# Kernel optimization log

Hardware: AMD Instinct MI355X
Metric: run time of the kernel (lower is better)

The kernel has to match this reference:

```python
import jax, jax.numpy as jnp
import numpy as np

N, E, D = 50000, 600000, 128

def _lin(key, fan_in, fan_out):
    kw, kb = jax.random.split(key)
    s = 1.0 / np.sqrt(fan_in)
    W = jax.random.uniform(kw, (fan_in, fan_out), minval=-s, maxval=s, dtype=jnp.float32)
    b = jax.random.uniform(kb, (fan_out,), minval=-s, maxval=s, dtype=jnp.float32)
    return W, b

def setup_inputs() -> dict:
    key = jax.random.key(0)
    ks = jax.random.split(key, 16)
    h = jax.random.normal(ks[0], (N, D), dtype=jnp.float32)
    pos = jax.random.normal(ks[1], (N, 2), dtype=jnp.float32)
    edge_index = jax.random.randint(ks[2], (2, E), 0, N, dtype=jnp.int64)
    edge_attr = jax.random.uniform(ks[3], (E, 1), dtype=jnp.float32)
    Wq, bq = _lin(ks[4], D, D)
    Wk, bk = _lin(ks[5], D, D)
    Wv, bv = _lin(ks[6], D, D)
    We1, be1 = _lin(ks[7], 1, D)
    We2, be2 = _lin(ks[8], D, D)
    Wa1, ba1 = _lin(ks[9], 3 * D, D)
    Wa2, ba2 = _lin(ks[10], D, 1)
    Wm1, bm1 = _lin(ks[11], 2 * D, D)
    Wm2, bm2 = _lin(ks[12], D, D)
    return dict(h=h, pos=pos, edge_index=edge_index, edge_attr=edge_attr,
                Wq=Wq, bq=bq, Wk=Wk, bk=bk, Wv=Wv, bv=bv,
                We1=We1, be1=be1, We2=We2, be2=be2,
                Wa1=Wa1, ba1=ba1, Wa2=Wa2, ba2=ba2,
                Wm1=Wm1, bm1=bm1, Wm2=Wm2, bm2=bm2)

def reference(h, pos, edge_index, edge_attr,
              Wq, bq, Wk, bk, Wv, bv,
              We1, be1, We2, be2,
              Wa1, ba1, Wa2, ba2,
              Wm1, bm1, Wm2, bm2):
    row, col = edge_index[0], edge_index[1]  # source, destination
    q = h @ Wq + bq                          # [N, D]
    k = h @ Wk + bk
    v = h @ Wv + bv
    e = jax.nn.relu(edge_attr @ We1 + be1) @ We2 + be2  # [E, D]
    # per-edge attention logits
    attn_in = jnp.concatenate([q[col], k[row], e], axis=-1)          # [E, 3D]
    logits = (jax.nn.relu(attn_in @ Wa1 + ba1) @ Wa2 + ba2)[:, 0]    # [E]
    # segment softmax grouped by destination node (torch_geometric style)
    seg_max = jax.ops.segment_max(logits, col, num_segments=N)       # [N]
    ex = jnp.exp(logits - seg_max[col])
    seg_sum = jax.ops.segment_sum(ex, col, num_segments=N)           # [N]
    w = ex / (seg_sum[col] + 1e-16)                                  # [E]
    # per-edge messages
    msg_in = jnp.concatenate([v[row], e], axis=-1)                   # [E, 2D]
    msg = jax.nn.silu(msg_in @ Wm1 + bm1) @ Wm2 + bm2                # [E, D]
    agg = jax.ops.segment_sum(msg * w[:, None], col, num_segments=N) # [N, D]
    return (h + agg, pos)
```

## Files before the change

kernel.cpp:

```cpp
#include <hip/hip_runtime.h>
#include <math.h>

#define D 128
#define SB 256

typedef __attribute__((ext_vector_type(8))) short bf16x8;
typedef __attribute__((ext_vector_type(4))) float f32x4;

__device__ inline unsigned f2bf(float f) {
    unsigned u = __float_as_uint(f);
    return (u + 0x7FFFu + ((u >> 16) & 1u)) >> 16;
}

__global__ __launch_bounds__(256) void prep(
    const float* __restrict__ Wq, const float* __restrict__ bq,
    const float* __restrict__ Wk, const float* __restrict__ bk,
    const float* __restrict__ Wv, const float* __restrict__ bv,
    const float* __restrict__ Wa1, const float* __restrict__ ba1,
    const float* __restrict__ Wm1, const float* __restrict__ bm1,
    const float* __restrict__ We1, const float* __restrict__ be1,
    const float* __restrict__ We2, const float* __restrict__ be2,
    const float* __restrict__ Wm2,
    const int* __restrict__ ei, int E,
    ushort* __restrict__ Wpk, ushort* __restrict__ Wpk2,
    float* __restrict__ bqa, float* __restrict__ bka, float* __restrict__ bva,
    float* __restrict__ bounds,
    float2* __restrict__ AB, float2* __restrict__ MB,
    int* __restrict__ deg)
{
    __shared__ float smem[1536];
    int b = blockIdx.x;
    int t = threadIdx.x;
    int j = t & 127, half = t >> 7;
    if (b < 384) {
        int which = b >> 7, i = b & 127;
        const float *A, *B;
        if (which == 0)      { A = Wq; B = Wa1; }
        else if (which == 1) { A = Wk; B = Wa1 + 128 * D; }
        else                 { A = Wv; B = Wm1; }
        float acc = 0.f;
        for (int k = half * 64; k < half * 64 + 64; k++) acc += A[i * D + k] * B[k * D + j];
        smem[t] = acc;
        __syncthreads();
        if (half == 0) {
            float v = smem[j] + smem[128 + j];
            int gc = which * 128 + j;
            int nt = gc >> 4;
            int ks = i >> 5;
            int lane = (((i >> 3) & 3) << 4) | (gc & 15);
            int j8 = i & 7;
            Wpk[((nt * 4 + ks) * 64 + lane) * 8 + j8] = (ushort)f2bf(v);
        }
    } else if (b < 387) {
        int which = b - 384;
        const float *bias, *B, *extra; float *out;
        if (which == 0)      { bias = bq; B = Wa1;           out = bqa; extra = ba1; }
        else if (which == 1) { bias = bk; B = Wa1 + 128 * D; out = bka; extra = nullptr; }
        else                 { bias = bv; B = Wm1;           out = bva; extra = bm1; }
        float acc = 0.f;
        for (int k = half * 64; k < half * 64 + 64; k++) acc += bias[k] * B[k * D + j];
        smem[t] = acc;
        __syncthreads();
        if (half == 0) out[j] = smem[j] + smem[128 + j] + (extra ? extra[j] : 0.f);
    } else if (b == 387) {
        float* sb = smem;
        if (t < 128) {
            float w = We1[t], bb = be1[t];
            float th = (w != 0.f) ? (-bb / w) : 2.f;
            sb[t] = fminf(fmaxf(th, 0.f), 1.f);
        }
        __syncthreads();
        for (int k = 2; k <= 128; k <<= 1)
            for (int jj = k >> 1; jj > 0; jj >>= 1) {
                if (t < 128) {
                    int ixj = t ^ jj;
                    if (ixj > t) {
                        float a = sb[t], c = sb[ixj];
                        bool up = ((t & k) == 0);
                        if (up ? (a > c) : (a < c)) { sb[t] = c; sb[ixj] = a; }
                    }
                }
                __syncthreads();
            }
        if (t == 0) { bounds[0] = 0.f; bounds[129] = 1.f; }
        if (t < 128) bounds[1 + t] = sb[t];
    } else if (b < 517) {
        float* sb = smem;
        float* Ae = smem + 128;
        float* Be = smem + 256;
        float* P  = smem + 384;
        if (t < 128) {
            float w = We1[t], bb = be1[t];
            float th = (w != 0.f) ? (-bb / w) : 2.f;
            sb[t] = fminf(fmaxf(th, 0.f), 1.f);
        }
        __syncthreads();
        for (int k = 2; k <= 128; k <<= 1)
            for (int jj = k >> 1; jj > 0; jj >>= 1) {
                if (t < 128) {
                    int ixj = t ^ jj;
                    if (ixj > t) {
                        float a = sb[t], c = sb[ixj];
                        bool up = ((t & k) == 0);
                        if (up ? (a > c) : (a < c)) { sb[t] = c; sb[ixj] = a; }
                    }
                }
                __syncthreads();
            }
        int i = b - 388;
        float lo = (i == 0)   ? 0.f : sb[i - 1];
        float hi = (i == 128) ? 1.f : sb[i];
        float m = 0.5f * (lo + hi);
        float ae = 0.f, be = 0.f;
        for (int k = half * 64; k < half * 64 + 64; k++) {
            float ww = We1[k], bb2 = be1[k];
            if (m * ww + bb2 > 0.f) { ae += ww * We2[k * D + j]; be += bb2 * We2[k * D + j]; }
        }
        P[t] = ae; P[256 + t] = be;
        __syncthreads();
        if (half == 0) {
            Ae[j] = P[j] + P[128 + j];
            Be[j] = P[256 + j] + P[384 + j] + be2[j];
        }
        __syncthreads();
        float aa = 0.f, ba = 0.f, am = 0.f, bm = 0.f;
        for (int l2 = half * 64; l2 < half * 64 + 64; l2++) {
            float ael = Ae[l2], bel = Be[l2];
            float wa = Wa1[(256 + l2) * D + j];
            float wm = Wm1[(128 + l2) * D + j];
            aa += ael * wa; ba += bel * wa;
            am += ael * wm; bm += bel * wm;
        }
        P[t] = aa; P[256 + t] = ba; P[512 + t] = am; P[768 + t] = bm;
        __syncthreads();
        if (half == 0) {
            AB[i * 128 + j] = make_float2(P[j] + P[128 + j], P[256 + j] + P[384 + j]);
            MB[i * 128 + j] = make_float2(P[512 + j] + P[640 + j], P[768 + j] + P[896 + j]);
        }
    } else if (b < 645) {
        if (t < 128) {
            int i = b - 517;
            int nt = t >> 4;
            int ks = i >> 5;
            int lane = (((i >> 3) & 3) << 4) | (t & 15);
            int j8 = i & 7;
            Wpk2[((nt * 4 + ks) * 64 + lane) * 8 + j8] = (ushort)f2bf(Wm2[i * D + t]);
        }
    } else {
        int e = (b - 645) * 256 + t;
        if (e < E) atomicAdd(deg + ei[E + e], 1);
    }
}

__global__ __launch_bounds__(SB) void k_scan1(const int* __restrict__ deg, int N,
                                              int* __restrict__ partial)
{
    __shared__ int ls[SB];
    int t = threadIdx.x;
    int i = blockIdx.x * SB + t;
    ls[t] = (i < N) ? deg[i] : 0;
    __syncthreads();
    for (int s = SB / 2; s > 0; s >>= 1) {
        if (t < s) ls[t] += ls[t + s];
        __syncthreads();
    }
    if (t == 0) partial[blockIdx.x] = ls[0];
}

__global__ __launch_bounds__(SB) void k_scan23(const int* __restrict__ deg, int N,
                                               const int* __restrict__ partial, int NB,
                                               int* __restrict__ off)
{
    __shared__ int lp[SB];
    __shared__ int ls[SB];
    int t = threadIdx.x;
    int pv = (t < NB) ? partial[t] : 0;
    lp[t] = pv;
    __syncthreads();
    int pval = pv;
    for (int s = 1; s < SB; s <<= 1) {
        int add = (t >= s) ? lp[t - s] : 0;
        __syncthreads();
        pval += add;
        lp[t] = pval;
        __syncthreads();
    }
    int base = (blockIdx.x > 0) ? lp[blockIdx.x - 1] : 0;

    int i = blockIdx.x * SB + t;
    int v = (i < N) ? deg[i] : 0;
    ls[t] = v;
    __syncthreads();
    int val = v;
    for (int s = 1; s < SB; s <<= 1) {
        int add = (t >= s) ? ls[t - s] : 0;
        __syncthreads();
        val += add;
        ls[t] = val;
        __syncthreads();
    }
    if (i < N) off[i] = base + val - v;
}

__global__ __launch_bounds__(256) void k_scatter(const int* __restrict__ ei,
                                                 const float* __restrict__ eattr, int E,
                                                 const float* __restrict__ bounds,
                                                 int* __restrict__ off, int2* __restrict__ recs)
{
    __shared__ float bnd[130];
    int t = threadIdx.x;
    if (t < 130) bnd[t] = bounds[t];
    __syncthreads();
    int e = blockIdx.x * 256 + t;
    if (e >= E) return;
    int row = ei[e], col = ei[E + e];
    float a = eattr[e];
    int lo = 0, hi = 128;
    while (lo < hi) { int mid = (lo + hi + 1) >> 1; if (bnd[mid] <= a) lo = mid; else hi = mid - 1; }
    int p = atomicAdd(off + col, 1);
    recs[p] = make_int2(row | (lo << 17), __float_as_int(a));
}

__global__ __launch_bounds__(256) void node_gemm(
    const float* __restrict__ h, int N,
    const ushort* __restrict__ Wpk,
    const float* __restrict__ bqa, const float* __restrict__ bka, const float* __restrict__ bva,
    ushort* __restrict__ qb, unsigned* __restrict__ kv)
{
    __shared__ __align__(16) ushort hsb[64 * 128];
    int t = threadIdx.x;
    int row0 = blockIdx.x * 64;
#pragma unroll
    for (int i = 0; i < 4; i++) {
        int g = t + i * 256;
        int r = g >> 4, c = g & 15;
        int grow = row0 + r;
        float4 f0, f1;
        if (grow < N) {
            const float4* hp = (const float4*)(h + (size_t)grow * D + c * 8);
            f0 = hp[0]; f1 = hp[1];
        } else {
            f0 = make_float4(0.f, 0.f, 0.f, 0.f); f1 = f0;
        }
        ushort u[8] = { (ushort)f2bf(f0.x), (ushort)f2bf(f0.y), (ushort)f2bf(f0.z), (ushort)f2bf(f0.w),
                        (ushort)f2bf(f1.x), (ushort)f2bf(f1.y), (ushort)f2bf(f1.z), (ushort)f2bf(f1.w) };
        int pc = c ^ (r & 15);
        *(uint4*)&hsb[r * 128 + pc * 8] = *(uint4*)u;
    }
    __syncthreads();

    int w = t >> 6, l = t & 63;
    int lrow = w * 16 + (l & 15);
    f32x4 acc[24];
#pragma unroll
    for (int i = 0; i < 24; i++) acc[i] = (f32x4){0.f, 0.f, 0.f, 0.f};

    const bf16x8* WB = (const bf16x8*)Wpk;
#pragma unroll
    for (int ks = 0; ks < 4; ks++) {
        int c = (ks * 4 + (l >> 4)) ^ (l & 15);
        bf16x8 afrag = *(const bf16x8*)&hsb[lrow * 128 + c * 8];
#pragma unroll
        for (int nt = 0; nt < 24; nt++) {
            bf16x8 bfrag = WB[(nt * 4 + ks) * 64 + l];
            acc[nt] = __builtin_amdgcn_mfma_f32_16x16x32_bf16(afrag, bfrag, acc[nt], 0, 0, 0);
        }
    }

    int rbase = row0 + w * 16 + ((l >> 4) << 2);
    int cl = l & 15;
#pragma unroll
    for (int cc = 0; cc < 8; cc++) {
        float bqv = bqa[cc * 16 + cl];
        float bkv = bka[cc * 16 + cl];
        float bvv = bva[cc * 16 + cl];
        f32x4 aq = acc[cc], ak = acc[8 + cc], av = acc[16 + cc];
#pragma unroll
        for (int r = 0; r < 4; r++) {
            int row = rbase + r;
            if (row < N) {
                qb[(size_t)row * D + cc * 16 + cl] = (ushort)f2bf(aq[r] + bqv);
                kv[(size_t)row * D + cc * 16 + cl] =
                    (f2bf(av[r] + bvv) << 16) | f2bf(ak[r] + bkv);
            }
        }
    }
}

__global__ __launch_bounds__(256) void node_all(
    const int2* __restrict__ recs, int N,
    const int* __restrict__ off,
    const ushort* __restrict__ qb, const unsigned* __restrict__ kv,
    const float2* __restrict__ AB, const float2* __restrict__ MB,
    const float* __restrict__ Wa2,
    unsigned* __restrict__ Sb, float* __restrict__ segsum)
{
    int t = threadIdx.x;
    int l = t & 31;
    int n = blockIdx.x * 8 + (t >> 5);
    bool valid = (n < N);
    int start = 0, end = 0;
    if (valid) {
        end = off[n];
        start = (n > 0) ? off[n - 1] : 0;
    }

    const char* kvc = (const char*)kv;
    const char* ABc = (const char*)AB;
    const char* MBc = (const char*)MB;

    uint2 qp = valid ? *(const uint2*)(qb + (size_t)n * D + 4 * l) : make_uint2(0u, 0u);
    float q0 = __uint_as_float(qp.x << 16);
    float q1 = __uint_as_float(qp.x & 0xFFFF0000u);
    float q2 = __uint_as_float(qp.y << 16);
    float q3 = __uint_as_float(qp.y & 0xFFFF0000u);
    float4 w4 = *(const float4*)(Wa2 + 4 * l);

    float m_run = -INFINITY;
    float a0 = 0.f, a1 = 0.f, a2 = 0.f, a3 = 0.f, ssum = 0.f;

    int idx = start;
    for (; idx + 2 <= end; idx += 2) {
        int2 rec1 = recs[idx];
        int2 rec2 = recs[idx + 1];
        unsigned u1 = (unsigned)rec1.x, u2 = (unsigned)rec2.x;
        float at1 = __int_as_float(rec1.y), at2 = __int_as_float(rec2.y);
        int rb1 = (int)(u1 & 0x1FFFFu) << 9, tb1 = (int)(u1 >> 17) << 10;
        int rb2 = (int)(u2 & 0x1FFFFu) << 9, tb2 = (int)(u2 >> 17) << 10;

        uint4 kp1 = *(const uint4*)(kvc + rb1 + (l << 4));
        uint4 kp2 = *(const uint4*)(kvc + rb2 + (l << 4));
        float4 ab0a = *(const float4*)(ABc + tb1 + (l << 5));
        float4 ab1a = *(const float4*)(ABc + tb1 + (l << 5) + 16);
        float4 mb0a = *(const float4*)(MBc + tb1 + (l << 5));
        float4 mb1a = *(const float4*)(MBc + tb1 + (l << 5) + 16);
        float4 ab0b = *(const float4*)(ABc + tb2 + (l << 5));
        float4 ab1b = *(const float4*)(ABc + tb2 + (l << 5) + 16);
        float4 mb0b = *(const float4*)(MBc + tb2 + (l << 5));
        float4 mb1b = *(const float4*)(MBc + tb2 + (l << 5) + 16);

        float p1 = fmaxf(q0 + __uint_as_float(kp1.x << 16) + at1 * ab0a.x + ab0a.y, 0.f) * w4.x
                 + fmaxf(q1 + __uint_as_float(kp1.y << 16) + at1 * ab0a.z + ab0a.w, 0.f) * w4.y
                 + fmaxf(q2 + __uint_as_float(kp1.z << 16) + at1 * ab1a.x + ab1a.y, 0.f) * w4.z
                 + fmaxf(q3 + __uint_as_float(kp1.w << 16) + at1 * ab1a.z + ab1a.w, 0.f) * w4.w;
        float p2 = fmaxf(q0 + __uint_as_float(kp2.x << 16) + at2 * ab0b.x + ab0b.y, 0.f) * w4.x
                 + fmaxf(q1 + __uint_as_float(kp2.y << 16) + at2 * ab0b.z + ab0b.w, 0.f) * w4.y
                 + fmaxf(q2 + __uint_as_float(kp2.z << 16) + at2 * ab1b.x + ab1b.y, 0.f) * w4.z
                 + fmaxf(q3 + __uint_as_float(kp2.w << 16) + at2 * ab1b.z + ab1b.w, 0.f) * w4.w;
#pragma unroll
        for (int s = 1; s < 32; s <<= 1) {
            p1 += __shfl_xor(p1, s, 64);
            p2 += __shfl_xor(p2, s, 64);
        }
        float d1 = p1 - m_run, d2 = p2 - m_run;
        if (fmaxf(d1, d2) > 8.f) {
            float mN = fmaxf(fmaxf(p1, p2), m_run);
            float sc = __expf(m_run - mN);
            a0 *= sc; a1 *= sc; a2 *= sc; a3 *= sc; ssum *= sc;
            m_run = mN; d1 = p1 - mN; d2 = p2 - mN;
        }
        float ex1 = __expf(d1), ex2 = __expf(d2);

        float x0 = __uint_as_float(kp1.x & 0xFFFF0000u) + at1 * mb0a.x + mb0a.y;
        float x1 = __uint_as_float(kp1.y & 0xFFFF0000u) + at1 * mb0a.z + mb0a.w;
        float x2 = __uint_as_float(kp1.z & 0xFFFF0000u) + at1 * mb1a.x + mb1a.y;
        float x3 = __uint_as_float(kp1.w & 0xFFFF0000u) + at1 * mb1a.z + mb1a.w;
        float y0 = __uint_as_float(kp2.x & 0xFFFF0000u) + at2 * mb0b.x + mb0b.y;
        float y1 = __uint_as_float(kp2.y & 0xFFFF0000u) + at2 * mb0b.z + mb0b.w;
        float y2 = __uint_as_float(kp2.z & 0xFFFF0000u) + at2 * mb1b.x + mb1b.y;
        float y3 = __uint_as_float(kp2.w & 0xFFFF0000u) + at2 * mb1b.z + mb1b.w;
        float s10 = x0 * __builtin_amdgcn_rcpf(1.f + __expf(-x0));
        float s11 = x1 * __builtin_amdgcn_rcpf(1.f + __expf(-x1));
        float s12 = x2 * __builtin_amdgcn_rcpf(1.f + __expf(-x2));
        float s13 = x3 * __builtin_amdgcn_rcpf(1.f + __expf(-x3));
        float s20 = y0 * __builtin_amdgcn_rcpf(1.f + __expf(-y0));
        float s21 = y1 * __builtin_amdgcn_rcpf(1.f + __expf(-y1));
        float s22 = y2 * __builtin_amdgcn_rcpf(1.f + __expf(-y2));
        float s23 = y3 * __builtin_amdgcn_rcpf(1.f + __expf(-y3));

        a0 = fmaf(ex2, s20, fmaf(ex1, s10, a0));
        a1 = fmaf(ex2, s21, fmaf(ex1, s11, a1));
        a2 = fmaf(ex2, s22, fmaf(ex1, s12, a2));
        a3 = fmaf(ex2, s23, fmaf(ex1, s13, a3));
        ssum += ex1 + ex2;
    }
    if (idx < end) {
        int2 rec = recs[idx];
        unsigned u1 = (unsigned)rec.x;
        float a = __int_as_float(rec.y);
        int rb = (int)(u1 & 0x1FFFFu) << 9, tb = (int)(u1 >> 17) << 10;
        uint4 kp = *(const uint4*)(kvc + rb + (l << 4));
        float4 ab0 = *(const float4*)(ABc + tb + (l << 5));
        float4 ab1 = *(const float4*)(ABc + tb + (l << 5) + 16);
        float4 mb0 = *(const float4*)(MBc + tb + (l << 5));
        float4 mb1 = *(const float4*)(MBc + tb + (l << 5) + 16);
        float p1 = fmaxf(q0 + __uint_as_float(kp.x << 16) + a * ab0.x + ab0.y, 0.f) * w4.x
                 + fmaxf(q1 + __uint_as_float(kp.y << 16) + a * ab0.z + ab0.w, 0.f) * w4.y
                 + fmaxf(q2 + __uint_as_float(kp.z << 16) + a * ab1.x + ab1.y, 0.f) * w4.z
                 + fmaxf(q3 + __uint_as_float(kp.w << 16) + a * ab1.z + ab1.w, 0.f) * w4.w;
#pragma unroll
        for (int s = 1; s < 32; s <<= 1) p1 += __shfl_xor(p1, s, 64);
        float d1 = p1 - m_run;
        if (d1 > 8.f) {
            float mN = p1;
            float sc = __expf(m_run - mN);
            a0 *= sc; a1 *= sc; a2 *= sc; a3 *= sc; ssum *= sc;
            m_run = mN; d1 = 0.f;
        }
        float ex = __expf(d1);
        float x0 = __uint_as_float(kp.x & 0xFFFF0000u) + a * mb0.x + mb0.y;
        float x1 = __uint_as_float(kp.y & 0xFFFF0000u) + a * mb0.z + mb0.w;
        float x2 = __uint_as_float(kp.z & 0xFFFF0000u) + a * mb1.x + mb1.y;
        float x3 = __uint_as_float(kp.w & 0xFFFF0000u) + a * mb1.z + mb1.w;
        a0 = fmaf(ex, x0 * __builtin_amdgcn_rcpf(1.f + __expf(-x0)), a0);
        a1 = fmaf(ex, x1 * __builtin_amdgcn_rcpf(1.f + __expf(-x1)), a1);
        a2 = fmaf(ex, x2 * __builtin_amdgcn_rcpf(1.f + __expf(-x2)), a2);
        a3 = fmaf(ex, x3 * __builtin_amdgcn_rcpf(1.f + __expf(-x3)), a3);
        ssum += ex;
    }

    if (valid) {
        float inv = __builtin_amdgcn_rcpf(ssum + 1e-16f);
        unsigned pw0 = f2bf(a0 * inv) | (f2bf(a1 * inv) << 16);
        unsigned pw1 = f2bf(a2 * inv) | (f2bf(a3 * inv) << 16);
        *(uint2*)(Sb + (size_t)n * 64 + 2 * l) = make_uint2(pw0, pw1);
        if (l == 0) segsum[n] = ssum;
    }
}

__global__ __launch_bounds__(256) void node_out(
    const float* __restrict__ h, int N,
    const unsigned* __restrict__ Sb, const ushort* __restrict__ Wpk2,
    const float* __restrict__ bm2, const float* __restrict__ segsum,
    float* __restrict__ out, const float* __restrict__ pos, int npos, int G1)
{
    int b = blockIdx.x;
    int t = threadIdx.x;
    if (b >= G1) {
        int i = ((b - G1) * 256 + t) * 4;
        float* outp = out + (size_t)N * D;
        if (i + 3 < npos) {
            *(float4*)(outp + i) = *(const float4*)(pos + i);
        } else {
            for (int j = i; j < npos; j++) outp[j] = pos[j];
        }
        return;
    }
    __shared__ __align__(16) ushort ssb[64 * 128];
    int row0 = b * 64;
#pragma unroll
    for (int i = 0; i < 4; i++) {
        int g = t + i * 256;
        int r = g >> 4, c = g & 15;
        int grow = row0 + r;
        uint4 u = make_uint4(0u, 0u, 0u, 0u);
        if (grow < N) u = *(const uint4*)(Sb + (size_t)grow * 64 + c * 4);
        int pc = c ^ (r & 15);
        *(uint4*)&ssb[r * 128 + pc * 8] = u;
    }
    __syncthreads();

    int w = t >> 6, l = t & 63;
    int lrow = w * 16 + (l & 15);
    f32x4 acc[8];
#pragma unroll
    for (int i = 0; i < 8; i++) acc[i] = (f32x4){0.f, 0.f, 0.f, 0.f};

    const bf16x8* WB = (const bf16x8*)Wpk2;
#pragma unroll
    for (int ks = 0; ks < 4; ks++) {
        int c = (ks * 4 + (l >> 4)) ^ (l & 15);
        bf16x8 afrag = *(const bf16x8*)&ssb[lrow * 128 + c * 8];
#pragma unroll
        for (int nt = 0; nt < 8; nt++) {
            bf16x8 bfrag = WB[(nt * 4 + ks) * 64 + l];
            acc[nt] = __builtin_amdgcn_mfma_f32_16x16x32_bf16(afrag, bfrag, acc[nt], 0, 0, 0);
        }
    }

    int rbase = row0 + w * 16 + ((l >> 4) << 2);
    int cl = l & 15;
#pragma unroll
    for (int cc = 0; cc < 8; cc++) {
        float bb = bm2[cc * 16 + cl];
        f32x4 av = acc[cc];
#pragma unroll
        for (int r = 0; r < 4; r++) {
            int row = rbase + r;
            if (row < N) {
                float ws_ = segsum[row];
                ws_ = ws_ / (ws_ + 1e-16f);
                out[(size_t)row * D + cc * 16 + cl] =
                    h[(size_t)row * D + cc * 16 + cl] + av[r] + bb * ws_;
            }
        }
    }
}

extern "C" void kernel_launch(void* const* d_in, const int* in_sizes, int n_in,
                              void* d_out, int out_size, void* d_ws, size_t ws_size,
                              hipStream_t stream)
{
    const float* h     = (const float*)d_in[0];
    const float* pos   = (const float*)d_in[1];
    const int*   ei    = (const int*)d_in[2];
    const float* eattr = (const float*)d_in[3];
    const float* Wq  = (const float*)d_in[4];  const float* bq  = (const float*)d_in[5];
    const float* Wk  = (const float*)d_in[6];  const float* bk  = (const float*)d_in[7];
    const float* Wv  = (const float*)d_in[8];  const float* bv  = (const float*)d_in[9];
    const float* We1 = (const float*)d_in[10]; const float* be1 = (const float*)d_in[11];
    const float* We2 = (const float*)d_in[12]; const float* be2 = (const float*)d_in[13];
    const float* Wa1 = (const float*)d_in[14]; const float* ba1 = (const float*)d_in[15];
    const float* Wa2 = (const float*)d_in[16];
    const float* Wm1 = (const float*)d_in[18]; const float* bm1 = (const float*)d_in[19];
    const float* Wm2 = (const float*)d_in[20]; const float* bm2 = (const float*)d_in[21];

    int N = in_sizes[0] / D;
    int E = in_sizes[3];
    int NB = (N + SB - 1) / SB;

    float* ws = (float*)d_ws;
    size_t off_f = 0;
    auto alloc = [&](size_t n) { float* p = ws + off_f; off_f += (n + 63) & ~(size_t)63; return p; };

    ushort* Wpk  = (ushort*)alloc(24 * 4 * 64 * 8 / 2);
    ushort* Wpk2 = (ushort*)alloc(8 * 4 * 64 * 8 / 2);
    float* bqa = alloc(D); float* bka = alloc(D); float* bva = alloc(D);
    float* bounds = alloc(130);
    float2* AB = (float2*)alloc((size_t)129 * 128 * 2);
    float2* MB = (float2*)alloc((size_t)129 * 128 * 2);
    ushort* qb = (ushort*)alloc((size_t)N * 64);
    unsigned* kv = (unsigned*)alloc((size_t)N * D);
    unsigned* Sb = (unsigned*)alloc((size_t)N * 64);
    float* segsum = alloc(N);
    int* deg  = (int*)alloc(N);
    int* offs = (int*)alloc(N);
    int* partial = (int*)alloc(256);
    int2* recs = (int2*)alloc((size_t)E * 2);

    hipMemsetAsync(deg, 0, (size_t)N * 4, stream);

    int HB = (E + 255) / 256;
    prep<<<645 + HB, 256, 0, stream>>>(Wq, bq, Wk, bk, Wv, bv, Wa1, ba1, Wm1, bm1,
                                       We1, be1, We2, be2, Wm2, ei, E,
                                       Wpk, Wpk2, bqa, bka, bva, bounds, AB, MB, deg);

    k_scan1<<<NB, SB, 0, stream>>>(deg, N, partial);
    k_scan23<<<NB, SB, 0, stream>>>(deg, N, partial, NB, offs);

    node_gemm<<<(N + 63) / 64, 256, 0, stream>>>(h, N, Wpk, bqa, bka, bva, qb, kv);

    k_scatter<<<(E + 255) / 256, 256, 0, stream>>>(ei, eattr, E, bounds, offs, recs);

    node_all<<<(N + 7) / 8, 256, 0, stream>>>(recs, N, offs, qb, kv, AB, MB, Wa2,
                                              Sb, segsum);

    int G1 = (N + 63) / 64;
    int G2 = (2 * N + 1023) / 1024;
    node_out<<<G1 + G2, 256, 0, stream>>>(h, N, Sb, Wpk2, bm2, segsum, (float*)d_out,
                                          pos, 2 * N, G1);
}
```

Measured before the change: 245.2 us.

## Sort nodes by in-degree so each node_all block handles similar-degree nodes

Builds a 64-bin in-degree histogram during the first scan pass. The second scan pass uses it to build a node permutation grouped by degree, and node_all processes nodes in that order. The aim is to cut warp and block imbalance, where one high-degree node leaves the other warps in a block idle. The cost is global atomics per node on 64 counters and a serial prefix in one thread per block. It also breaks node locality for reads of qb and off and for writes of Sb and segsum.

```diff
diff --git a/kernel.cpp b/kernel.cpp
--- a/kernel.cpp
+++ b/kernel.cpp
@@ -153,12 +153,15 @@
 }
 
 __global__ __launch_bounds__(SB) void k_scan1(const int* __restrict__ deg, int N,
-                                              int* __restrict__ partial)
+                                              int* __restrict__ partial,
+                                              int* __restrict__ binH)
 {
     __shared__ int ls[SB];
     int t = threadIdx.x;
     int i = blockIdx.x * SB + t;
-    ls[t] = (i < N) ? deg[i] : 0;
+    int v = (i < N) ? deg[i] : 0;
+    ls[t] = v;
+    if (i < N) atomicAdd(binH + (v < 63 ? v : 63), 1);
     __syncthreads();
     for (int s = SB / 2; s > 0; s >>= 1) {
         if (t < s) ls[t] += ls[t + s];
@@ -169,13 +172,21 @@
 
 __global__ __launch_bounds__(SB) void k_scan23(const int* __restrict__ deg, int N,
                                                const int* __restrict__ partial, int NB,
+                                               const int* __restrict__ binH,
+                                               int* __restrict__ binCur,
+                                               int* __restrict__ nodePerm,
                                                int* __restrict__ off)
 {
     __shared__ int lp[SB];
     __shared__ int ls[SB];
+    __shared__ int bse[64];
     int t = threadIdx.x;
     int pv = (t < NB) ? partial[t] : 0;
     lp[t] = pv;
+    if (t == 0) {
+        int run = 0;
+        for (int b2 = 0; b2 < 64; b2++) { bse[b2] = run; run += binH[b2]; }
+    }
     __syncthreads();
     int pval = pv;
     for (int s = 1; s < SB; s <<= 1) {
@@ -199,7 +210,12 @@
         ls[t] = val;
         __syncthreads();
     }
-    if (i < N) off[i] = base + val - v;
+    if (i < N) {
+        off[i] = base + val - v;
+        int bidx = (v < 63 ? v : 63);
+        int pos = bse[bidx] + atomicAdd(binCur + bidx, 1);
+        nodePerm[pos] = i;
+    }
 }
 
 __global__ __launch_bounds__(256) void k_scatter(const int* __restrict__ ei,
@@ -289,7 +305,7 @@
 
 __global__ __launch_bounds__(256) void node_all(
     const int2* __restrict__ recs, int N,
-    const int* __restrict__ off,
+    const int* __restrict__ off, const int* __restrict__ nodePerm,
     const ushort* __restrict__ qb, const unsigned* __restrict__ kv,
     const float2* __restrict__ AB, const float2* __restrict__ MB,
     const float* __restrict__ Wa2,
@@ -297,8 +313,9 @@
 {
     int t = threadIdx.x;
     int l = t & 31;
-    int n = blockIdx.x * 8 + (t >> 5);
-    bool valid = (n < N);
+    int n0 = blockIdx.x * 8 + (t >> 5);
+    bool valid = (n0 < N);
+    int n = valid ? nodePerm[n0] : 0;
     int start = 0, end = 0;
     if (valid) {
         end = off[n];
@@ -533,26 +550,29 @@
     unsigned* kv = (unsigned*)alloc((size_t)N * D);
     unsigned* Sb = (unsigned*)alloc((size_t)N * 64);
     float* segsum = alloc(N);
-    int* deg  = (int*)alloc(N);
+    int* deg  = (int*)alloc(N + 128);
+    int* binH = deg + N;
+    int* binCur = deg + N + 64;
     int* offs = (int*)alloc(N);
+    int* nodePerm = (int*)alloc(N);
     int* partial = (int*)alloc(256);
     int2* recs = (int2*)alloc((size_t)E * 2);
 
-    hipMemsetAsync(deg, 0, (size_t)N * 4, stream);
+    hipMemsetAsync(deg, 0, ((size_t)N + 128) * 4, stream);
 
     int HB = (E + 255) / 256;
     prep<<<645 + HB, 256, 0, stream>>>(Wq, bq, Wk, bk, Wv, bv, Wa1, ba1, Wm1, bm1,
                                        We1, be1, We2, be2, Wm2, ei, E,
                                        Wpk, Wpk2, bqa, bka, bva, bounds, AB, MB, deg);
 
-    k_scan1<<<NB, SB, 0, stream>>>(deg, N, partial);
-    k_scan23<<<NB, SB, 0, stream>>>(deg, N, partial, NB, offs);
+    k_scan1<<<NB, SB, 0, stream>>>(deg, N, partial, binH);
+    k_scan23<<<NB, SB, 0, stream>>>(deg, N, partial, NB, binH, binCur, nodePerm, offs);
 
     node_gemm<<<(N + 63) / 64, 256, 0, stream>>>(h, N, Wpk, bqa, bka, bva, qb, kv);
 
     k_scatter<<<(E + 255) / 256, 256, 0, stream>>>(ei, eattr, E, bounds, offs, recs);
 
-    node_all<<<(N + 7) / 8, 256, 0, stream>>>(recs, N, offs, qb, kv, AB, MB, Wa2,
+    node_all<<<(N + 7) / 8, 256, 0, stream>>>(recs, N, offs, nodePerm, qb, kv, AB, MB, Wa2,
                                               Sb, segsum);
 
     int G1 = (N + 63) / 64;
```

Result: slower. 546.7 us (+123.0%).
